# Kernel optimization log

Hardware: AMD Instinct MI355X
Metric: run time of the kernel (lower is better)

The kernel has to match this reference:

```python
import jax, jax.numpy as jnp
import numpy as np

N_HEAD = 16
D_HEAD = 64
HIDDEN = 1024
T = 2048
B = 4


def setup_inputs() -> dict:
    key = jax.random.key(0)
    k1, k2, k3, k4, k5 = jax.random.split(key, 5)
    qkv_out = (2 * N_HEAD + 1) * D_HEAD  # 2112
    return {
        "x": jax.random.normal(k1, (B, T, HIDDEN), dtype=jnp.float32),
        "w_qkv": jax.random.normal(k2, (qkv_out, HIDDEN), dtype=jnp.float32) * (HIDDEN ** -0.5),
        "b_qkv": jax.random.normal(k3, (qkv_out,), dtype=jnp.float32) * 0.02,
        "w_out": jax.random.normal(k4, (HIDDEN, D_HEAD), dtype=jnp.float32) * (D_HEAD ** -0.5),
        "b_out": jax.random.normal(k5, (HIDDEN,), dtype=jnp.float32) * 0.02,
    }


def reference(x, w_qkv, b_qkv, w_out, b_out):
    bs, t, h = x.shape
    scale = D_HEAD ** -0.5
    qkv = x @ w_qkv.T + b_qkv  # [b, t, (2H+1)*dh]
    q, k, v = jnp.split(qkv, [N_HEAD * D_HEAD, 2 * N_HEAD * D_HEAD], axis=-1)
    q = q.reshape(bs, t, N_HEAD, D_HEAD)
    k = k.reshape(bs, t, N_HEAD, D_HEAD)
    v = v.reshape(bs, t, D_HEAD)  # single V head shared across all heads
    # attn_score: [b, h, i, j]
    attn_score = jnp.einsum("bihd,bjhd->bhij", q, k) * scale
    # causal mask: -inf above diagonal
    causal = jnp.triu(jnp.full((t, t), -jnp.inf, dtype=attn_score.dtype), 1)
    attn_score = attn_score + causal
    attn_prob = jax.nn.softmax(attn_score, axis=-1)  # dropout is identity in eval
    # shared V across heads: [b,h,i,j] x [b,j,d] -> [b,h,i,d]
    attn_vec = jnp.einsum("bhij,bjd->bhid", attn_prob, v)
    m_attn_vec = jnp.mean(attn_vec, axis=1)  # mean over heads -> [b, t, d_head]
    out = m_attn_vec @ w_out.T + b_out  # [b, t, hidden]
    return out, attn_vec
```

## Files before the change

kernel.cpp:

```cpp
#include <hip/hip_runtime.h>
#include <hip/hip_bf16.h>
#include <math.h>

#define NHEAD 16
#define DHEAD 64
#define HIDDEN 1024
#define TSEQ 2048
#define BATCH 4
#define QKV_OUT 2112
#define BT (BATCH * TSEQ)

typedef __attribute__((ext_vector_type(8))) short bf16x8;
typedef __attribute__((ext_vector_type(4))) float floatx4;

static __device__ __forceinline__ short f2bf(float x) {
  __hip_bfloat16 h = __float2bfloat16(x);
  return *reinterpret_cast<short*>(&h);
}

__global__ __launch_bounds__(256) void f32_to_bf16(
    const float* __restrict__ src, short* __restrict__ dst, int n) {
  const int i = (blockIdx.x * 256 + threadIdx.x) * 8;
  if (i >= n) return;
  float4 a = *(const float4*)&src[i];
  float4 b = *(const float4*)&src[i + 4];
  short o[8];
  o[0] = f2bf(a.x); o[1] = f2bf(a.y); o[2] = f2bf(a.z); o[3] = f2bf(a.w);
  o[4] = f2bf(b.x); o[5] = f2bf(b.y); o[6] = f2bf(b.z); o[7] = f2bf(b.w);
  *(uint4*)&dst[i] = *(uint4*)o;
}

#define QK_BM 128
#define QK_BN 64
#define QK_BK 64

template <typename OUT_T>
__global__ __launch_bounds__(256) void gemm_mfma_bf16(
    const short* __restrict__ A, const short* __restrict__ B,
    const float* __restrict__ bias, OUT_T* __restrict__ C,
    int M, int N, int K) {
  __shared__ short As[QK_BM][72];
  __shared__ short Bs[QK_BN][72];

  const int tid = threadIdx.x;
  const int lane = tid & 63;
  const int wv = tid >> 6;
  const int ln = lane & 15;
  const int grp = lane >> 4;
  const int wm = wv >> 1;
  const int wn = wv & 1;
  const int rowbase = blockIdx.y * QK_BM;
  const int colbase = blockIdx.x * QK_BN;

  const int ar = tid >> 1, ac = (tid & 1) * 32;
  const int br = tid >> 2, bc = (tid & 3) * 16;

  floatx4 acc[4][2];
#pragma unroll
  for (int m = 0; m < 4; ++m)
#pragma unroll
    for (int n = 0; n < 2; ++n) acc[m][n] = (floatx4){0.f, 0.f, 0.f, 0.f};

  for (int k0 = 0; k0 < K; k0 += QK_BK) {
    const short* ap = A + (size_t)(rowbase + ar) * K + k0 + ac;
    uint4 a0 = *(const uint4*)(ap + 0);
    uint4 a1 = *(const uint4*)(ap + 8);
    uint4 a2 = *(const uint4*)(ap + 16);
    uint4 a3 = *(const uint4*)(ap + 24);
    const short* bp = B + (size_t)(colbase + br) * K + k0 + bc;
    uint4 b0 = *(const uint4*)(bp + 0);
    uint4 b1 = *(const uint4*)(bp + 8);
    __syncthreads();
    *(uint4*)&As[ar][ac + 0] = a0;
    *(uint4*)&As[ar][ac + 8] = a1;
    *(uint4*)&As[ar][ac + 16] = a2;
    *(uint4*)&As[ar][ac + 24] = a3;
    *(uint4*)&Bs[br][bc + 0] = b0;
    *(uint4*)&Bs[br][bc + 8] = b1;
    __syncthreads();

#pragma unroll
    for (int ks = 0; ks < 2; ++ks) {
      bf16x8 bfrag[2];
#pragma unroll
      for (int n = 0; n < 2; ++n)
        bfrag[n] = *(const bf16x8*)&Bs[wn * 32 + n * 16 + ln][ks * 32 + grp * 8];
#pragma unroll
      for (int m = 0; m < 4; ++m) {
        bf16x8 af = *(const bf16x8*)&As[wm * 64 + m * 16 + ln][ks * 32 + grp * 8];
#pragma unroll
        for (int n = 0; n < 2; ++n)
          acc[m][n] = __builtin_amdgcn_mfma_f32_16x16x32_bf16(af, bfrag[n], acc[m][n], 0, 0, 0);
      }
    }
  }

#pragma unroll
  for (int n = 0; n < 2; ++n) {
    const int col = colbase + wn * 32 + n * 16 + ln;
    const float bv = bias[col];
#pragma unroll
    for (int m = 0; m < 4; ++m) {
#pragma unroll
      for (int r = 0; r < 4; ++r) {
        const int row = rowbase + wm * 64 + m * 16 + grp * 4 + r;
        const float v = acc[m][n][r] + bv;
        if constexpr (sizeof(OUT_T) == 2)
          C[(size_t)row * N + col] = f2bf(v);
        else
          C[(size_t)row * N + col] = v;
      }
    }
  }
}

__global__ __launch_bounds__(256) void transpose_v(
    const short* __restrict__ qkv, short* __restrict__ vt) {
  __shared__ short tile[64][72];
  const int tt = blockIdx.x;
  const int b = blockIdx.y;
  const int tid = threadIdx.x;
  const int li = tid >> 2;
  const int lc = (tid & 3) * 16;

  const short* src = qkv + (size_t)(b * TSEQ + tt * 64 + li) * QKV_OUT + 2048 + lc;
  *(uint4*)&tile[li][lc] = *(const uint4*)src;
  *(uint4*)&tile[li][lc + 8] = *(const uint4*)(src + 8);
  __syncthreads();
  short tmp[16];
#pragma unroll
  for (int u = 0; u < 16; ++u) tmp[u] = tile[lc + u][li];
  short* dst = vt + (size_t)(b * 64 + li) * TSEQ + tt * 64 + lc;
  *(uint4*)dst = *(uint4*)&tmp[0];
  *(uint4*)(dst + 8) = *(uint4*)&tmp[8];
}

__global__ __launch_bounds__(256) void attn_kernel(
    const short* __restrict__ qkv, const short* __restrict__ vt,
    float* __restrict__ attn_vec) {
  __shared__ short Ks[64][72];
  __shared__ short Vt[64][72];
  __shared__ short Ps[64][72];

  const int tid = threadIdx.x;
  const int it = gridDim.x - 1 - blockIdx.x;
  const int h = blockIdx.y;
  const int b = blockIdx.z;
  const int lane = tid & 63;
  const int wv = tid >> 6;
  const int ln = lane & 15;
  const int grp = lane >> 4;
  const int qbase = wv * 16;
  const int sli = tid & 63;
  const int slc = (tid >> 6) * 16;
  const float CEXP = 0.18033688f;

  const short* qptr = qkv + (size_t)(b * TSEQ + it * 64 + qbase + ln) * QKV_OUT + h * 64;
  const bf16x8 bq0 = *(const bf16x8*)(qptr + grp * 8);
  const bf16x8 bq1 = *(const bf16x8*)(qptr + 32 + grp * 8);

  floatx4 oT[4];
#pragma unroll
  for (int m = 0; m < 4; ++m) oT[m] = (floatx4){0.f, 0.f, 0.f, 0.f};
  float l = 0.f;

  const int njt = it + 1;
  const short* ks0 = qkv + (size_t)(b * TSEQ + sli) * QKV_OUT + 1024 + h * 64 + slc;
  const short* vs0 = vt + (size_t)(b * 64 + sli) * TSEQ + slc;
  uint4 kr0 = *(const uint4*)ks0;
  uint4 kr1 = *(const uint4*)(ks0 + 8);
  uint4 vr0 = *(const uint4*)vs0;
  uint4 vr1 = *(const uint4*)(vs0 + 8);

  for (int jt = 0; jt < njt; ++jt) {
    __syncthreads();
    *(uint4*)&Ks[sli][slc] = kr0;
    *(uint4*)&Ks[sli][slc + 8] = kr1;
    *(uint4*)&Vt[sli][slc] = vr0;
    *(uint4*)&Vt[sli][slc + 8] = vr1;
    __syncthreads();

    if (jt + 1 < njt) {
      const short* kn = qkv + (size_t)(b * TSEQ + (jt + 1) * 64 + sli) * QKV_OUT + 1024 + h * 64 + slc;
      const short* vn = vt + (size_t)(b * 64 + sli) * TSEQ + (jt + 1) * 64 + slc;
      kr0 = *(const uint4*)kn;
      kr1 = *(const uint4*)(kn + 8);
      vr0 = *(const uint4*)vn;
      vr1 = *(const uint4*)(vn + 8);
    }

    floatx4 st[4];
#pragma unroll
    for (int m = 0; m < 4; ++m) {
      bf16x8 ak0 = *(const bf16x8*)&Ks[m * 16 + ln][grp * 8];
      bf16x8 ak1 = *(const bf16x8*)&Ks[m * 16 + ln][32 + grp * 8];
      floatx4 a = (floatx4){0.f, 0.f, 0.f, 0.f};
      a = __builtin_amdgcn_mfma_f32_16x16x32_bf16(ak0, bq0, a, 0, 0, 0);
      a = __builtin_amdgcn_mfma_f32_16x16x32_bf16(ak1, bq1, a, 0, 0, 0);
      st[m] = a;
    }

    if (jt == it) {
#pragma unroll
      for (int m = 0; m < 4; ++m)
#pragma unroll
        for (int r = 0; r < 4; ++r)
          if (m * 16 + grp * 4 + r > qbase + ln) st[m][r] = -INFINITY;
    }

#pragma unroll
    for (int m = 0; m < 4; ++m) {
      float p0 = exp2f(CEXP * st[m][0]);
      float p1 = exp2f(CEXP * st[m][1]);
      float p2 = exp2f(CEXP * st[m][2]);
      float p3 = exp2f(CEXP * st[m][3]);
      l += (p0 + p1) + (p2 + p3);
      short pk[4] = {f2bf(p0), f2bf(p1), f2bf(p2), f2bf(p3)};
      *(uint2*)&Ps[qbase + ln][m * 16 + grp * 4] = *(uint2*)pk;
    }

    bf16x8 bp0 = *(const bf16x8*)&Ps[qbase + ln][grp * 8];
    bf16x8 bp1 = *(const bf16x8*)&Ps[qbase + ln][32 + grp * 8];
#pragma unroll
    for (int m = 0; m < 4; ++m) {
      bf16x8 av0 = *(const bf16x8*)&Vt[m * 16 + ln][grp * 8];
      bf16x8 av1 = *(const bf16x8*)&Vt[m * 16 + ln][32 + grp * 8];
      oT[m] = __builtin_amdgcn_mfma_f32_16x16x32_bf16(av0, bp0, oT[m], 0, 0, 0);
      oT[m] = __builtin_amdgcn_mfma_f32_16x16x32_bf16(av1, bp1, oT[m], 0, 0, 0);
    }
  }

  l += __shfl_xor(l, 16);
  l += __shfl_xor(l, 32);
  const float inv = 1.f / l;

  float* orow = attn_vec + ((size_t)(b * NHEAD + h) * TSEQ + it * 64 + qbase + ln) * DHEAD;
#pragma unroll
  for (int m = 0; m < 4; ++m) {
    float4 o4;
    o4.x = oT[m][0] * inv;
    o4.y = oT[m][1] * inv;
    o4.z = oT[m][2] * inv;
    o4.w = oT[m][3] * inv;
    *(float4*)&orow[m * 16 + grp * 4] = o4;
  }
}

__global__ __launch_bounds__(256) void mean_heads(
    const float* __restrict__ attn_vec, short* __restrict__ m) {
  const int gid = blockIdx.x * 256 + threadIdx.x;
  const int d2 = (gid & 31) * 2;
  const int t = (gid >> 5) & (TSEQ - 1);
  const int b = gid >> 16;
  float s0 = 0.f, s1 = 0.f;
#pragma unroll
  for (int h = 0; h < NHEAD; ++h) {
    const float* p = &attn_vec[(((size_t)(b * NHEAD + h) * TSEQ) + t) * DHEAD + d2];
    s0 += p[0];
    s1 += p[1];
  }
  short pk[2] = {f2bf(s0 * (1.f / 16.f)), f2bf(s1 * (1.f / 16.f))};
  *(uint*)&m[gid * 2] = *(uint*)pk;
}

extern "C" void kernel_launch(void* const* d_in, const int* in_sizes, int n_in,
                              void* d_out, int out_size, void* d_ws, size_t ws_size,
                              hipStream_t stream) {
  const float* x     = (const float*)d_in[0];
  const float* w_qkv = (const float*)d_in[1];
  const float* b_qkv = (const float*)d_in[2];
  const float* w_out = (const float*)d_in[3];
  const float* b_out = (const float*)d_in[4];

  float* out      = (float*)d_out;
  float* attn_vec = out + (size_t)BT * HIDDEN;

  short* qkv_bf  = (short*)d_ws;
  short* vt_bf   = qkv_bf + (size_t)BT * QKV_OUT;
  short* x_bf    = vt_bf + (size_t)BATCH * DHEAD * TSEQ;
  short* w_bf    = x_bf + (size_t)BT * HIDDEN;
  short* wout_bf = w_bf + (size_t)QKV_OUT * HIDDEN;
  short* m_attn  = wout_bf + (size_t)HIDDEN * DHEAD;

  f32_to_bf16<<<dim3(BT * HIDDEN / 8 / 256), 256, 0, stream>>>(
      x, x_bf, BT * HIDDEN);
  f32_to_bf16<<<dim3(QKV_OUT * HIDDEN / 8 / 256), 256, 0, stream>>>(
      w_qkv, w_bf, QKV_OUT * HIDDEN);
  f32_to_bf16<<<dim3(HIDDEN * DHEAD / 8 / 256), 256, 0, stream>>>(
      w_out, wout_bf, HIDDEN * DHEAD);

  gemm_mfma_bf16<short><<<dim3(QKV_OUT / QK_BN, BT / QK_BM), 256, 0, stream>>>(
      x_bf, w_bf, b_qkv, qkv_bf, BT, QKV_OUT, HIDDEN);

  transpose_v<<<dim3(TSEQ / 64, BATCH), 256, 0, stream>>>(qkv_bf, vt_bf);

  attn_kernel<<<dim3(TSEQ / 64, NHEAD, BATCH), 256, 0, stream>>>(
      qkv_bf, vt_bf, attn_vec);

  mean_heads<<<dim3(BT * DHEAD / 2 / 256), 256, 0, stream>>>(attn_vec, m_attn);

  gemm_mfma_bf16<float><<<dim3(HIDDEN / QK_BN, BT / QK_BM), 256, 0, stream>>>(
      m_attn, wout_bf, b_out, out, BT, HIDDEN, DHEAD);
}
```

Measured before the change: 313.9 us.

## Process two 64-query subtiles per attention block to share K/V tiles

Each attention block now handles 128 query rows, split into two 64-row subtiles, and reuses every staged K and V tile for both. This halves global and LDS staging traffic per query and halves the number of blocks launched. The first subtile skips its work past its own causal diagonal. The single P buffer is reused for both subtiles, and the extra accumulators raise register pressure, which may lower occupancy.

```diff
diff --git a/kernel.cpp b/kernel.cpp
--- a/kernel.cpp
+++ b/kernel.cpp
@@ -17,6 +17,8 @@
   __hip_bfloat16 h = __float2bfloat16(x);
   return *reinterpret_cast<short*>(&h);
 }
+
+#define MFMA16(a, b, c) __builtin_amdgcn_mfma_f32_16x16x32_bf16(a, b, c, 0, 0, 0)
 
 __global__ __launch_bounds__(256) void f32_to_bf16(
     const float* __restrict__ src, short* __restrict__ dst, int n) {
@@ -90,7 +92,7 @@
         bf16x8 af = *(const bf16x8*)&As[wm * 64 + m * 16 + ln][ks * 32 + grp * 8];
 #pragma unroll
         for (int n = 0; n < 2; ++n)
-          acc[m][n] = __builtin_amdgcn_mfma_f32_16x16x32_bf16(af, bfrag[n], acc[m][n], 0, 0, 0);
+          acc[m][n] = MFMA16(af, bfrag[n], acc[m][n]);
       }
     }
   }
@@ -143,28 +145,39 @@
   __shared__ short Ps[64][72];
 
   const int tid = threadIdx.x;
-  const int it = gridDim.x - 1 - blockIdx.x;
+  const int itb = gridDim.x - 1 - blockIdx.x;
   const int h = blockIdx.y;
   const int b = blockIdx.z;
   const int lane = tid & 63;
   const int wv = tid >> 6;
   const int ln = lane & 15;
   const int grp = lane >> 4;
-  const int qbase = wv * 16;
   const int sli = tid & 63;
   const int slc = (tid >> 6) * 16;
   const float CEXP = 0.18033688f;
-
-  const short* qptr = qkv + (size_t)(b * TSEQ + it * 64 + qbase + ln) * QKV_OUT + h * 64;
-  const bf16x8 bq0 = *(const bf16x8*)(qptr + grp * 8);
-  const bf16x8 bq1 = *(const bf16x8*)(qptr + 32 + grp * 8);
-
-  floatx4 oT[4];
-#pragma unroll
-  for (int m = 0; m < 4; ++m) oT[m] = (floatx4){0.f, 0.f, 0.f, 0.f};
-  float l = 0.f;
-
-  const int njt = it + 1;
+  const int q0 = itb * 128;
+
+  bf16x8 bq[2][2];
+#pragma unroll
+  for (int s = 0; s < 2; ++s) {
+    const short* qptr =
+        qkv + (size_t)(b * TSEQ + q0 + s * 64 + wv * 16 + ln) * QKV_OUT + h * 64;
+    bq[s][0] = *(const bf16x8*)(qptr + grp * 8);
+    bq[s][1] = *(const bf16x8*)(qptr + 32 + grp * 8);
+  }
+
+  floatx4 oT[2][4];
+#pragma unroll
+  for (int s = 0; s < 2; ++s)
+#pragma unroll
+    for (int m = 0; m < 4; ++m) oT[s][m] = (floatx4){0.f, 0.f, 0.f, 0.f};
+  float lsum[2] = {0.f, 0.f};
+
+  const int njt = 2 * itb + 2;
+  {
+    const short* ks0 = qkv + (size_t)(b * TSEQ + sli) * QKV_OUT + 1024 + h * 64 + slc;
+    const short* vs0 = vt + (size_t)(b * 64 + sli) * TSEQ + slc;
+  }
   const short* ks0 = qkv + (size_t)(b * TSEQ + sli) * QKV_OUT + 1024 + h * 64 + slc;
   const short* vs0 = vt + (size_t)(b * 64 + sli) * TSEQ + slc;
   uint4 kr0 = *(const uint4*)ks0;
@@ -181,7 +194,8 @@
     __syncthreads();
 
     if (jt + 1 < njt) {
-      const short* kn = qkv + (size_t)(b * TSEQ + (jt + 1) * 64 + sli) * QKV_OUT + 1024 + h * 64 + slc;
+      const short* kn =
+          qkv + (size_t)(b * TSEQ + (jt + 1) * 64 + sli) * QKV_OUT + 1024 + h * 64 + slc;
       const short* vn = vt + (size_t)(b * 64 + sli) * TSEQ + (jt + 1) * 64 + slc;
       kr0 = *(const uint4*)kn;
       kr1 = *(const uint4*)(kn + 8);
@@ -189,60 +203,96 @@
       vr1 = *(const uint4*)(vn + 8);
     }
 
-    floatx4 st[4];
+    const bool act0 = (jt <= 2 * itb);
+
+    floatx4 st[2][4];
 #pragma unroll
     for (int m = 0; m < 4; ++m) {
       bf16x8 ak0 = *(const bf16x8*)&Ks[m * 16 + ln][grp * 8];
       bf16x8 ak1 = *(const bf16x8*)&Ks[m * 16 + ln][32 + grp * 8];
-      floatx4 a = (floatx4){0.f, 0.f, 0.f, 0.f};
-      a = __builtin_amdgcn_mfma_f32_16x16x32_bf16(ak0, bq0, a, 0, 0, 0);
-      a = __builtin_amdgcn_mfma_f32_16x16x32_bf16(ak1, bq1, a, 0, 0, 0);
-      st[m] = a;
-    }
-
-    if (jt == it) {
-#pragma unroll
-      for (int m = 0; m < 4; ++m)
-#pragma unroll
-        for (int r = 0; r < 4; ++r)
-          if (m * 16 + grp * 4 + r > qbase + ln) st[m][r] = -INFINITY;
-    }
-
-#pragma unroll
-    for (int m = 0; m < 4; ++m) {
-      float p0 = exp2f(CEXP * st[m][0]);
-      float p1 = exp2f(CEXP * st[m][1]);
-      float p2 = exp2f(CEXP * st[m][2]);
-      float p3 = exp2f(CEXP * st[m][3]);
-      l += (p0 + p1) + (p2 + p3);
-      short pk[4] = {f2bf(p0), f2bf(p1), f2bf(p2), f2bf(p3)};
-      *(uint2*)&Ps[qbase + ln][m * 16 + grp * 4] = *(uint2*)pk;
-    }
-
-    bf16x8 bp0 = *(const bf16x8*)&Ps[qbase + ln][grp * 8];
-    bf16x8 bp1 = *(const bf16x8*)&Ps[qbase + ln][32 + grp * 8];
+      if (act0) {
+        floatx4 a = (floatx4){0.f, 0.f, 0.f, 0.f};
+        a = MFMA16(ak0, bq[0][0], a);
+        a = MFMA16(ak1, bq[0][1], a);
+        st[0][m] = a;
+      }
+      floatx4 a1 = (floatx4){0.f, 0.f, 0.f, 0.f};
+      a1 = MFMA16(ak0, bq[1][0], a1);
+      a1 = MFMA16(ak1, bq[1][1], a1);
+      st[1][m] = a1;
+    }
+
+#pragma unroll
+    for (int s = 0; s < 2; ++s) {
+      if (jt == 2 * itb + s) {
+#pragma unroll
+        for (int m = 0; m < 4; ++m)
+#pragma unroll
+          for (int r = 0; r < 4; ++r)
+            if (m * 16 + grp * 4 + r > wv * 16 + ln) st[s][m][r] = -INFINITY;
+      }
+    }
+
+    bf16x8 bp[2][2];
+    if (act0) {
+#pragma unroll
+      for (int m = 0; m < 4; ++m) {
+        float p0 = exp2f(CEXP * st[0][m][0]);
+        float p1 = exp2f(CEXP * st[0][m][1]);
+        float p2 = exp2f(CEXP * st[0][m][2]);
+        float p3 = exp2f(CEXP * st[0][m][3]);
+        lsum[0] += (p0 + p1) + (p2 + p3);
+        short pk[4] = {f2bf(p0), f2bf(p1), f2bf(p2), f2bf(p3)};
+        *(uint2*)&Ps[wv * 16 + ln][m * 16 + grp * 4] = *(uint2*)pk;
+      }
+      bp[0][0] = *(const bf16x8*)&Ps[wv * 16 + ln][grp * 8];
+      bp[0][1] = *(const bf16x8*)&Ps[wv * 16 + ln][32 + grp * 8];
+    }
+    {
+#pragma unroll
+      for (int m = 0; m < 4; ++m) {
+        float p0 = exp2f(CEXP * st[1][m][0]);
+        float p1 = exp2f(CEXP * st[1][m][1]);
+        float p2 = exp2f(CEXP * st[1][m][2]);
+        float p3 = exp2f(CEXP * st[1][m][3]);
+        lsum[1] += (p0 + p1) + (p2 + p3);
+        short pk[4] = {f2bf(p0), f2bf(p1), f2bf(p2), f2bf(p3)};
+        *(uint2*)&Ps[wv * 16 + ln][m * 16 + grp * 4] = *(uint2*)pk;
+      }
+      bp[1][0] = *(const bf16x8*)&Ps[wv * 16 + ln][grp * 8];
+      bp[1][1] = *(const bf16x8*)&Ps[wv * 16 + ln][32 + grp * 8];
+    }
+
 #pragma unroll
     for (int m = 0; m < 4; ++m) {
       bf16x8 av0 = *(const bf16x8*)&Vt[m * 16 + ln][grp * 8];
       bf16x8 av1 = *(const bf16x8*)&Vt[m * 16 + ln][32 + grp * 8];
-      oT[m] = __builtin_amdgcn_mfma_f32_16x16x32_bf16(av0, bp0, oT[m], 0, 0, 0);
-      oT[m] = __builtin_amdgcn_mfma_f32_16x16x32_bf16(av1, bp1, oT[m], 0, 0, 0);
-    }
-  }
-
-  l += __shfl_xor(l, 16);
-  l += __shfl_xor(l, 32);
-  const float inv = 1.f / l;
-
-  float* orow = attn_vec + ((size_t)(b * NHEAD + h) * TSEQ + it * 64 + qbase + ln) * DHEAD;
-#pragma unroll
-  for (int m = 0; m < 4; ++m) {
-    float4 o4;
-    o4.x = oT[m][0] * inv;
-    o4.y = oT[m][1] * inv;
-    o4.z = oT[m][2] * inv;
-    o4.w = oT[m][3] * inv;
-    *(float4*)&orow[m * 16 + grp * 4] = o4;
+      if (act0) {
+        oT[0][m] = MFMA16(av0, bp[0][0], oT[0][m]);
+        oT[0][m] = MFMA16(av1, bp[0][1], oT[0][m]);
+      }
+      oT[1][m] = MFMA16(av0, bp[1][0], oT[1][m]);
+      oT[1][m] = MFMA16(av1, bp[1][1], oT[1][m]);
+    }
+  }
+
+#pragma unroll
+  for (int s = 0; s < 2; ++s) {
+    float l = lsum[s];
+    l += __shfl_xor(l, 16);
+    l += __shfl_xor(l, 32);
+    const float inv = 1.f / l;
+    float* orow =
+        attn_vec + ((size_t)(b * NHEAD + h) * TSEQ + q0 + s * 64 + wv * 16 + ln) * DHEAD;
+#pragma unroll
+    for (int m = 0; m < 4; ++m) {
+      float4 o4;
+      o4.x = oT[s][m][0] * inv;
+      o4.y = oT[s][m][1] * inv;
+      o4.z = oT[s][m][2] * inv;
+      o4.w = oT[s][m][3] * inv;
+      *(float4*)&orow[m * 16 + grp * 4] = o4;
+    }
   }
 }
 
@@ -294,7 +344,7 @@
 
   transpose_v<<<dim3(TSEQ / 64, BATCH), 256, 0, stream>>>(qkv_bf, vt_bf);
 
-  attn_kernel<<<dim3(TSEQ / 64, NHEAD, BATCH), 256, 0, stream>>>(
+  attn_kernel<<<dim3(TSEQ / 128, NHEAD, BATCH), 256, 0, stream>>>(
       qkv_bf, vt_bf, attn_vec);
 
   mean_heads<<<dim3(BT * DHEAD / 2 / 256), 256, 0, stream>>>(attn_vec, m_attn);
```

After: 313.1 us. No clear change (-0.3%).

## Split causal attention KV range into chunks with partial-sum combine kernel

Applied to the files above, without the earlier changes.

Query tiles are split along the key dimension into chunks of 8 key tiles, so later query tiles get up to 4 blocks instead of one long serial loop. This balances work across CUs. Because the softmax uses no running max, the partial outputs and row sums are written to workspace and added in a separate combine kernel. The cost is an extra launch and about 75MB of fp32 partial traffic. The workspace is aliased over the x/w bf16 buffers, which are dead by the time attention runs.

```diff
diff --git a/kernel.cpp b/kernel.cpp
--- a/kernel.cpp
+++ b/kernel.cpp
@@ -17,6 +17,8 @@
   __hip_bfloat16 h = __float2bfloat16(x);
   return *reinterpret_cast<short*>(&h);
 }
+
+#define MFMA16(a, b, c) __builtin_amdgcn_mfma_f32_16x16x32_bf16(a, b, c, 0, 0, 0)
 
 __global__ __launch_bounds__(256) void f32_to_bf16(
     const float* __restrict__ src, short* __restrict__ dst, int n) {
@@ -90,7 +92,7 @@
         bf16x8 af = *(const bf16x8*)&As[wm * 64 + m * 16 + ln][ks * 32 + grp * 8];
 #pragma unroll
         for (int n = 0; n < 2; ++n)
-          acc[m][n] = __builtin_amdgcn_mfma_f32_16x16x32_bf16(af, bfrag[n], acc[m][n], 0, 0, 0);
+          acc[m][n] = MFMA16(af, bfrag[n], acc[m][n]);
       }
     }
   }
@@ -135,15 +137,31 @@
   *(uint4*)(dst + 8) = *(uint4*)&tmp[8];
 }
 
-__global__ __launch_bounds__(256) void attn_kernel(
+#define CH 8
+
+__global__ __launch_bounds__(256) void attn_partial(
     const short* __restrict__ qkv, const short* __restrict__ vt,
-    float* __restrict__ attn_vec) {
+    float* __restrict__ attn_vec, float* __restrict__ pO,
+    float* __restrict__ pL) {
   __shared__ short Ks[64][72];
   __shared__ short Vt[64][72];
   __shared__ short Ps[64][72];
 
+  const int x = gridDim.x - 1 - blockIdx.x;
+  int it, jc;
+  if (x < 8) {
+    it = x; jc = 0;
+  } else if (x < 24) {
+    it = 8 + ((x - 8) >> 1); jc = (x - 8) & 1;
+  } else if (x < 48) {
+    it = 16 + (x - 24) / 3; jc = (x - 24) % 3;
+  } else {
+    it = 24 + ((x - 48) >> 2); jc = (x - 48) & 3;
+  }
+  const int jstart = jc * CH;
+  const int jend = min(jstart + CH, it + 1);
+
   const int tid = threadIdx.x;
-  const int it = gridDim.x - 1 - blockIdx.x;
   const int h = blockIdx.y;
   const int b = blockIdx.z;
   const int lane = tid & 63;
@@ -162,17 +180,16 @@
   floatx4 oT[4];
 #pragma unroll
   for (int m = 0; m < 4; ++m) oT[m] = (floatx4){0.f, 0.f, 0.f, 0.f};
-  float l = 0.f;
-
-  const int njt = it + 1;
-  const short* ks0 = qkv + (size_t)(b * TSEQ + sli) * QKV_OUT + 1024 + h * 64 + slc;
-  const short* vs0 = vt + (size_t)(b * 64 + sli) * TSEQ + slc;
+  float lsum = 0.f;
+
+  const short* ks0 = qkv + (size_t)(b * TSEQ + jstart * 64 + sli) * QKV_OUT + 1024 + h * 64 + slc;
+  const short* vs0 = vt + (size_t)(b * 64 + sli) * TSEQ + jstart * 64 + slc;
   uint4 kr0 = *(const uint4*)ks0;
   uint4 kr1 = *(const uint4*)(ks0 + 8);
   uint4 vr0 = *(const uint4*)vs0;
   uint4 vr1 = *(const uint4*)(vs0 + 8);
 
-  for (int jt = 0; jt < njt; ++jt) {
+  for (int jt = jstart; jt < jend; ++jt) {
     __syncthreads();
     *(uint4*)&Ks[sli][slc] = kr0;
     *(uint4*)&Ks[sli][slc + 8] = kr1;
@@ -180,8 +197,9 @@
     *(uint4*)&Vt[sli][slc + 8] = vr1;
     __syncthreads();
 
-    if (jt + 1 < njt) {
-      const short* kn = qkv + (size_t)(b * TSEQ + (jt + 1) * 64 + sli) * QKV_OUT + 1024 + h * 64 + slc;
+    if (jt + 1 < jend) {
+      const short* kn =
+          qkv + (size_t)(b * TSEQ + (jt + 1) * 64 + sli) * QKV_OUT + 1024 + h * 64 + slc;
       const short* vn = vt + (size_t)(b * 64 + sli) * TSEQ + (jt + 1) * 64 + slc;
       kr0 = *(const uint4*)kn;
       kr1 = *(const uint4*)(kn + 8);
@@ -195,8 +213,8 @@
       bf16x8 ak0 = *(const bf16x8*)&Ks[m * 16 + ln][grp * 8];
       bf16x8 ak1 = *(const bf16x8*)&Ks[m * 16 + ln][32 + grp * 8];
       floatx4 a = (floatx4){0.f, 0.f, 0.f, 0.f};
-      a = __builtin_amdgcn_mfma_f32_16x16x32_bf16(ak0, bq0, a, 0, 0, 0);
-      a = __builtin_amdgcn_mfma_f32_16x16x32_bf16(ak1, bq1, a, 0, 0, 0);
+      a = MFMA16(ak0, bq0, a);
+      a = MFMA16(ak1, bq1, a);
       st[m] = a;
     }
 
@@ -214,7 +232,7 @@
       float p1 = exp2f(CEXP * st[m][1]);
       float p2 = exp2f(CEXP * st[m][2]);
       float p3 = exp2f(CEXP * st[m][3]);
-      l += (p0 + p1) + (p2 + p3);
+      lsum += (p0 + p1) + (p2 + p3);
       short pk[4] = {f2bf(p0), f2bf(p1), f2bf(p2), f2bf(p3)};
       *(uint2*)&Ps[qbase + ln][m * 16 + grp * 4] = *(uint2*)pk;
     }
@@ -225,24 +243,79 @@
     for (int m = 0; m < 4; ++m) {
       bf16x8 av0 = *(const bf16x8*)&Vt[m * 16 + ln][grp * 8];
       bf16x8 av1 = *(const bf16x8*)&Vt[m * 16 + ln][32 + grp * 8];
-      oT[m] = __builtin_amdgcn_mfma_f32_16x16x32_bf16(av0, bp0, oT[m], 0, 0, 0);
-      oT[m] = __builtin_amdgcn_mfma_f32_16x16x32_bf16(av1, bp1, oT[m], 0, 0, 0);
-    }
-  }
-
-  l += __shfl_xor(l, 16);
-  l += __shfl_xor(l, 32);
+      oT[m] = MFMA16(av0, bp0, oT[m]);
+      oT[m] = MFMA16(av1, bp1, oT[m]);
+    }
+  }
+
+  lsum += __shfl_xor(lsum, 16);
+  lsum += __shfl_xor(lsum, 32);
+
+  if (it < 8) {
+    const float inv = 1.f / lsum;
+    float* orow =
+        attn_vec + ((size_t)(b * NHEAD + h) * TSEQ + it * 64 + qbase + ln) * DHEAD;
+#pragma unroll
+    for (int m = 0; m < 4; ++m) {
+      float4 o4;
+      o4.x = oT[m][0] * inv;
+      o4.y = oT[m][1] * inv;
+      o4.z = oT[m][2] * inv;
+      o4.w = oT[m][3] * inv;
+      *(float4*)&orow[m * 16 + grp * 4] = o4;
+    }
+  } else {
+    const int slot = (it < 16) ? (it - 8) * 2 + jc
+                   : (it < 24) ? 16 + (it - 16) * 3 + jc
+                               : 40 + (it - 24) * 4 + jc;
+    const size_t sbase = (size_t)(b * NHEAD + h) * 72 + slot;
+    float* prow = pO + sbase * 4096 + (size_t)(qbase + ln) * 64;
+#pragma unroll
+    for (int m = 0; m < 4; ++m) {
+      float4 o4;
+      o4.x = oT[m][0]; o4.y = oT[m][1]; o4.z = oT[m][2]; o4.w = oT[m][3];
+      *(float4*)&prow[m * 16 + grp * 4] = o4;
+    }
+    if (grp == 0) pL[sbase * 64 + qbase + ln] = lsum;
+  }
+}
+
+__global__ __launch_bounds__(256) void attn_combine(
+    const float* __restrict__ pO, const float* __restrict__ pL,
+    float* __restrict__ attn_vec) {
+  const int it = 8 + blockIdx.x;
+  const int h = blockIdx.y;
+  const int b = blockIdx.z;
+  const int nch = (it < 16) ? 2 : (it < 24) ? 3 : 4;
+  const int slot0 = (it < 16) ? (it - 8) * 2
+                  : (it < 24) ? 16 + (it - 16) * 3
+                              : 40 + (it - 24) * 4;
+  const int q = threadIdx.x >> 2;
+  const int dbase = (threadIdx.x & 3) * 16;
+  const size_t base = (size_t)(b * NHEAD + h) * 72 + slot0;
+
+  float4 acc[4];
+#pragma unroll
+  for (int u = 0; u < 4; ++u) acc[u] = (float4){0.f, 0.f, 0.f, 0.f};
+  float l = 0.f;
+  for (int c = 0; c < nch; ++c) {
+    const float* pr = pO + (base + c) * 4096 + (size_t)q * 64 + dbase;
+#pragma unroll
+    for (int u = 0; u < 4; ++u) {
+      float4 v = *(const float4*)&pr[u * 4];
+      acc[u].x += v.x; acc[u].y += v.y; acc[u].z += v.z; acc[u].w += v.w;
+    }
+    l += pL[(base + c) * 64 + q];
+  }
   const float inv = 1.f / l;
-
-  float* orow = attn_vec + ((size_t)(b * NHEAD + h) * TSEQ + it * 64 + qbase + ln) * DHEAD;
-#pragma unroll
-  for (int m = 0; m < 4; ++m) {
+  float* orow =
+      attn_vec + ((size_t)(b * NHEAD + h) * TSEQ + it * 64 + q) * DHEAD + dbase;
+#pragma unroll
+  for (int u = 0; u < 4; ++u) {
     float4 o4;
-    o4.x = oT[m][0] * inv;
-    o4.y = oT[m][1] * inv;
-    o4.z = oT[m][2] * inv;
-    o4.w = oT[m][3] * inv;
-    *(float4*)&orow[m * 16 + grp * 4] = o4;
+    o4.x = acc[u].x * inv; o4.y = acc[u].y * inv;
+    o4.z = acc[u].z * inv; o4.w = acc[u].w * inv;
+    *(float4*)&orow[u * 4] = o4;
   }
 }
 
@@ -277,10 +350,13 @@
 
   short* qkv_bf  = (short*)d_ws;
   short* vt_bf   = qkv_bf + (size_t)BT * QKV_OUT;
-  short* x_bf    = vt_bf + (size_t)BATCH * DHEAD * TSEQ;
+  short* wout_bf = vt_bf + (size_t)BATCH * DHEAD * TSEQ;
+  short* m_attn  = wout_bf + (size_t)HIDDEN * DHEAD;
+  char*  xbase   = (char*)(m_attn + (size_t)BT * DHEAD);
+  short* x_bf    = (short*)xbase;
   short* w_bf    = x_bf + (size_t)BT * HIDDEN;
-  short* wout_bf = w_bf + (size_t)QKV_OUT * HIDDEN;
-  short* m_attn  = wout_bf + (size_t)HIDDEN * DHEAD;
+  float* pO      = (float*)xbase;
+  float* pL      = pO + (size_t)64 * 72 * 4096;
 
   f32_to_bf16<<<dim3(BT * HIDDEN / 8 / 256), 256, 0, stream>>>(
       x, x_bf, BT * HIDDEN);
@@ -294,8 +370,10 @@
 
   transpose_v<<<dim3(TSEQ / 64, BATCH), 256, 0, stream>>>(qkv_bf, vt_bf);
 
-  attn_kernel<<<dim3(TSEQ / 64, NHEAD, BATCH), 256, 0, stream>>>(
-      qkv_bf, vt_bf, attn_vec);
+  attn_partial<<<dim3(80, NHEAD, BATCH), 256, 0, stream>>>(
+      qkv_bf, vt_bf, attn_vec, pO, pL);
+
+  attn_combine<<<dim3(24, NHEAD, BATCH), 256, 0, stream>>>(pO, pL, attn_vec);
 
   mean_heads<<<dim3(BT * DHEAD / 2 / 256), 256, 0, stream>>>(attn_vec, m_attn);
 
```

After: 288.3 us. 8.2% less time.
